# Optimization experiments

Measured on AMD Instinct MI355X. Metric: run time of the kernel, lower is better.

Reference implementation:

```python
import jax, jax.numpy as jnp
import numpy as np

N_HEADS = 4
DIM_HEAD = 32


def setup_inputs() -> dict:
    key = jax.random.key(0)
    k1, k2, k3, k4 = jax.random.split(key, 4)
    x = jax.random.normal(k1, (8, 64, 80, 1024), dtype=jnp.float32)
    # conv_qkv: 1x1 conv, no bias -> weight [3*heads*dim_head, dim_in_out]
    w_qkv = jax.random.normal(k2, (3 * N_HEADS * DIM_HEAD, 64), dtype=jnp.float32) * 0.05
    # conv_out: 1x1 conv with bias -> weight [dim_in_out, heads*dim_head], bias [dim_in_out]
    w_out = jax.random.normal(k3, (64, N_HEADS * DIM_HEAD), dtype=jnp.float32) * 0.05
    b_out = jax.random.normal(k4, (64,), dtype=jnp.float32) * 0.05
    return {"x": x, "w_qkv": w_qkv, "w_out": w_out, "b_out": b_out}


def reference(x, w_qkv, w_out, b_out):
    b, c, h, w = x.shape
    n = h * w
    # 1x1 conv == channel matmul
    qkv = jnp.einsum('bchw,oc->bohw', x, w_qkv)            # [b, 3*heads*dh, h, w]
    qkv = qkv.reshape(b, 3, N_HEADS, DIM_HEAD, n)          # qkv outermost, then heads, then c
    q, k, v = qkv[:, 0], qkv[:, 1], qkv[:, 2]              # each [b, heads, dh, n]
    k = jax.nn.softmax(k, axis=-1)                          # softmax over spatial positions
    context = jnp.einsum('bhdn,bhen->bhde', k, v)          # [b, heads, dh, dh]
    out = jnp.einsum('bhde,bhdn->bhen', context, q)        # [b, heads, dh, n]
    out = out.reshape(b, N_HEADS * DIM_HEAD, h, w)
    return jnp.einsum('bchw,oc->bohw', out, w_out) + b_out[None, :, None, None]
```

## Files before the change

kernel.cpp:

```cpp
#include <hip/hip_runtime.h>
#include <stdint.h>


#define N_POS 81920
#define NT    64
#define TILES 1280

typedef short bf16x8 __attribute__((ext_vector_type(8)));
typedef float f32x4  __attribute__((ext_vector_type(4)));

__device__ __forceinline__ uint32_t packbf(float lo, float hi){
  uint32_t a = __float_as_uint(lo), b = __float_as_uint(hi);
  a = (a + 0x8000u) >> 16;
  b = (b + 0x8000u) & 0xffff0000u;
  return a | b;
}
__device__ __forceinline__ short bf16of(float v){
  return (short)((__float_as_uint(v) + 0x8000u) >> 16);
}

__global__ __launch_bounds__(512, 4) void kernA(
    const float* __restrict__ x, const float* __restrict__ w,
    float* __restrict__ pA, float* __restrict__ pZ, int nch, int tpc)
{
  __shared__ __align__(16) uint16_t xs_cp[64 * 72];
  __shared__ __align__(16) uint16_t xs_pc[64 * 72];
  __shared__ __align__(16) uint16_t es[128 * 72];

  const int t  = threadIdx.x;
  const int w8 = t >> 6;
  const int l  = t & 63;
  const int lm = l & 15;
  const int lg = l >> 4;

  const int b  = blockIdx.x / nch;
  const int ch = blockIdx.x % nch;
  const float* xb = x + (size_t)b * 64 * N_POS;

  const int sc  = t >> 3;
  const int spg = t & 7;
  const int spp = t & 63;
  const int scg = t >> 6;

  const int pt  = w8 & 3;
  const int ht0 = (w8 >> 2) * 4;

  bf16x8 wkf[4][2];
  #pragma unroll
  for (int i = 0; i < 4; ++i)
    #pragma unroll
    for (int kk = 0; kk < 2; ++kk){
      const float* wp = w + (size_t)(128 + 16*(ht0+i) + lm) * 64 + 32*kk + 8*lg;
      float4 w0 = *(const float4*)wp;
      float4 w1 = *(const float4*)(wp + 4);
      bf16x8 f;
      f[0]=bf16of(w0.x); f[1]=bf16of(w0.y); f[2]=bf16of(w0.z); f[3]=bf16of(w0.w);
      f[4]=bf16of(w1.x); f[5]=bf16of(w1.y); f[6]=bf16of(w1.z); f[7]=bf16of(w1.w);
      wkf[i][kk] = f;
    }

  bf16x8 ones;
  #pragma unroll
  for (int j = 0; j < 8; ++j) ones[j] = (short)0x3F80;

  f32x4 acc[4], zac;
  zac = (f32x4){0.f,0.f,0.f,0.f};
  #pragma unroll
  for (int n = 0; n < 4; ++n) acc[n] = (f32x4){0.f,0.f,0.f,0.f};

  float4 f0, f1;
  float v[8];
  {
    const int n0 = (ch * tpc) * NT;
    const float* ga = xb + (size_t)sc * N_POS + n0 + 8*spg;
    f0 = *(const float4*)ga;
    f1 = *(const float4*)(ga + 4);
    const float* gb = xb + (size_t)(8*scg) * N_POS + n0 + spp;
    #pragma unroll
    for (int i = 0; i < 8; ++i) v[i] = gb[(size_t)i * N_POS];
  }

  for (int tile = 0; tile < tpc; ++tile){
    __syncthreads();
    {
      uint4 u;
      u.x = packbf(f0.x,f0.y); u.y = packbf(f0.z,f0.w);
      u.z = packbf(f1.x,f1.y); u.w = packbf(f1.z,f1.w);
      *(uint4*)&xs_cp[sc*72 + 8*spg] = u;
      uint4 u2;
      u2.x = packbf(v[0],v[1]); u2.y = packbf(v[2],v[3]);
      u2.z = packbf(v[4],v[5]); u2.w = packbf(v[6],v[7]);
      *(uint4*)&xs_pc[spp*72 + 8*scg] = u2;
    }
    __syncthreads();
    if (tile + 1 < tpc){
      const int n1 = (ch * tpc + tile + 1) * NT;
      const float* ga = xb + (size_t)sc * N_POS + n1 + 8*spg;
      f0 = *(const float4*)ga;
      f1 = *(const float4*)(ga + 4);
      const float* gb = xb + (size_t)(8*scg) * N_POS + n1 + spp;
      #pragma unroll
      for (int i = 0; i < 8; ++i) v[i] = gb[(size_t)i * N_POS];
    }
    {
      bf16x8 af0 = *(const bf16x8*)&xs_pc[(16*pt + lm)*72 + 8*lg];
      bf16x8 af1 = *(const bf16x8*)&xs_pc[(16*pt + lm)*72 + 32 + 8*lg];
      #pragma unroll
      for (int i = 0; i < 4; ++i){
        f32x4 s = (f32x4){0.f,0.f,0.f,0.f};
        s = __builtin_amdgcn_mfma_f32_16x16x32_bf16(af0, wkf[i][0], s, 0,0,0);
        s = __builtin_amdgcn_mfma_f32_16x16x32_bf16(af1, wkf[i][1], s, 0,0,0);
        float e0 = __expf(s[0]), e1 = __expf(s[1]);
        float e2 = __expf(s[2]), e3 = __expf(s[3]);
        uint2 pk; pk.x = packbf(e0,e1); pk.y = packbf(e2,e3);
        *(uint2*)&es[(16*(ht0+i) + lm)*72 + 16*pt + 4*lg] = pk;
      }
    }
    __syncthreads();
    #pragma unroll
    for (int kk = 0; kk < 2; ++kk){
      bf16x8 ea = *(const bf16x8*)&es[(16*w8 + lm)*72 + 32*kk + 8*lg];
      bf16x8 xbf[4];
      #pragma unroll
      for (int n = 0; n < 4; ++n)
        xbf[n] = *(const bf16x8*)&xs_cp[(16*n + lm)*72 + 32*kk + 8*lg];
      #pragma unroll
      for (int n = 0; n < 4; ++n)
        acc[n] = __builtin_amdgcn_mfma_f32_16x16x32_bf16(ea, xbf[n], acc[n], 0,0,0);
      zac = __builtin_amdgcn_mfma_f32_16x16x32_bf16(ea, ones, zac, 0,0,0);
    }
  }

  float* pa = pA + (size_t)blockIdx.x * 8192;
  const int hd0 = 16*w8 + 4*lg;
  #pragma unroll
  for (int n = 0; n < 4; ++n)
    #pragma unroll
    for (int r = 0; r < 4; ++r)
      pa[(size_t)(hd0 + r)*64 + 16*n + lm] = acc[n][r];
  if (lm == 0){
    #pragma unroll
    for (int r = 0; r < 4; ++r)
      pZ[(size_t)blockIdx.x * 128 + hd0 + r] = zac[r];
  }
}

__global__ __launch_bounds__(256) void kernR1(
    const float* __restrict__ pA, const float* __restrict__ pZ,
    float* __restrict__ Ar, float* __restrict__ Zr, int nch)
{
  const int b = blockIdx.x >> 3, s = blockIdx.x & 7;
  const int off = s * 1024 + threadIdx.x * 4;
  float4 a = make_float4(0.f, 0.f, 0.f, 0.f);
  for (int ch = 0; ch < nch; ++ch){
    float4 v = *(const float4*)&pA[(size_t)(b * nch + ch) * 8192 + off];
    a.x += v.x; a.y += v.y; a.z += v.z; a.w += v.w;
  }
  *(float4*)&Ar[(size_t)b * 8192 + off] = a;
  if (s == 0 && threadIdx.x < 128){
    float z = 0.f;
    for (int ch = 0; ch < nch; ++ch) z += pZ[(size_t)(b * nch + ch) * 128 + threadIdx.x];
    Zr[b * 128 + threadIdx.x] = z;
  }
}

__global__ __launch_bounds__(256) void kernCM(
    const float* __restrict__ Ar, const float* __restrict__ Zr,
    const float* __restrict__ w_qkv, const float* __restrict__ w_out,
    float* __restrict__ M)
{
  __shared__ float A[128 * 65];
  __shared__ float Z[128];
  __shared__ float cs[128 * 33];
  __shared__ float T[64 * 129];
  const int b = blockIdx.x, t = threadIdx.x;

  #pragma unroll
  for (int k = 0; k < 32; ++k){
    int i = t + 256 * k;
    A[(i >> 6) * 65 + (i & 63)] = Ar[(size_t)b * 8192 + i];
  }
  if (t < 128) Z[t] = Zr[b * 128 + t];
  __syncthreads();

  {
    const int hd = t & 127, h = hd >> 5, e0 = (t >> 7) * 16;
    const float rz = 1.0f / Z[hd];
    for (int je = 0; je < 16; ++je){
      int e = e0 + je;
      const float* wv = w_qkv + (size_t)(256 + 32 * h + e) * 64;
      float a = 0.f;
      #pragma unroll
      for (int c = 0; c < 64; ++c) a = fmaf(A[hd * 65 + c], wv[c], a);
      cs[hd * 33 + e] = a * rz;
    }
  }
  __syncthreads();

  const int o = t & 63, g = t >> 6;
  for (int jh = 0; jh < 32; ++jh){
    int hd = 32 * g + jh;
    const float* wo = w_out + (size_t)o * 128 + 32 * g;
    float a = 0.f;
    #pragma unroll
    for (int e = 0; e < 32; ++e) a = fmaf(wo[e], cs[hd * 33 + e], a);
    T[o * 129 + hd] = a;
  }
  __syncthreads();

  const int c0 = 16 * g;
  float m[16];
  #pragma unroll
  for (int j = 0; j < 16; ++j) m[j] = 0.f;
  for (int hd = 0; hd < 128; ++hd){
    float tv = T[o * 129 + hd];
    const float* wq = w_qkv + (size_t)hd * 64 + c0;
    #pragma unroll
    for (int j = 0; j < 16; ++j) m[j] = fmaf(tv, wq[j], m[j]);
  }
  #pragma unroll
  for (int j = 0; j < 16; ++j) M[(size_t)b * 4096 + o * 64 + c0 + j] = m[j];
}

__global__ __launch_bounds__(256, 2) void kernO(
    const float* __restrict__ x, const float* __restrict__ M,
    const float* __restrict__ b_out, float* __restrict__ out)
{
  __shared__ __align__(16) uint16_t xs[256 * 72];

  const int t  = threadIdx.x;
  const int wv = t >> 6;
  const int l  = t & 63;
  const int lm = l & 15;
  const int lg = l >> 4;

  const int b  = blockIdx.x / 320;
  const int p0 = (blockIdx.x % 320) * 256;
  const float* xb = x + (size_t)b * 64 * N_POS + p0;

  const float* Mb = M + (size_t)b * 4096;
  bf16x8 mb[4][2];
  float bias[4];
  #pragma unroll
  for (int ot = 0; ot < 4; ++ot){
    bias[ot] = b_out[16*ot + lm];
    #pragma unroll
    for (int kk = 0; kk < 2; ++kk){
      const float* mp = Mb + (size_t)(16*ot + lm)*64 + 32*kk + 8*lg;
      float4 m0 = *(const float4*)mp;
      float4 m1 = *(const float4*)(mp + 4);
      bf16x8 f;
      f[0]=bf16of(m0.x); f[1]=bf16of(m0.y); f[2]=bf16of(m0.z); f[3]=bf16of(m0.w);
      f[4]=bf16of(m1.x); f[5]=bf16of(m1.y); f[6]=bf16of(m1.z); f[7]=bf16of(m1.w);
      mb[ot][kk] = f;
    }
  }

  #pragma unroll
  for (int cc = 0; cc < 8; ++cc){
    float v[8];
    #pragma unroll
    for (int j = 0; j < 8; ++j)
      v[j] = xb[(size_t)(8*cc + j) * N_POS + t];
    uint4 u;
    u.x = packbf(v[0],v[1]); u.y = packbf(v[2],v[3]);
    u.z = packbf(v[4],v[5]); u.w = packbf(v[6],v[7]);
    *(uint4*)&xs[t*72 + 8*cc] = u;
  }
  __syncthreads();

  float* ob = out + (size_t)b * 64 * N_POS + p0;

  #pragma unroll
  for (int ip = 0; ip < 4; ++ip){
    const int pt = 4*wv + ip;
    bf16x8 af0 = *(const bf16x8*)&xs[(16*pt + lm)*72 + 8*lg];
    bf16x8 af1 = *(const bf16x8*)&xs[(16*pt + lm)*72 + 32 + 8*lg];
    #pragma unroll
    for (int ot = 0; ot < 4; ++ot){
      f32x4 d = (f32x4){0.f,0.f,0.f,0.f};
      d = __builtin_amdgcn_mfma_f32_16x16x32_bf16(af0, mb[ot][0], d, 0,0,0);
      d = __builtin_amdgcn_mfma_f32_16x16x32_bf16(af1, mb[ot][1], d, 0,0,0);
      float4 st = make_float4(d[0]+bias[ot], d[1]+bias[ot],
                              d[2]+bias[ot], d[3]+bias[ot]);
      *(float4*)&ob[(size_t)(16*ot + lm) * N_POS + 16*pt + 4*lg] = st;
    }
  }
}

extern "C" void kernel_launch(void* const* d_in, const int* in_sizes, int n_in,
                              void* d_out, int out_size, void* d_ws, size_t ws_size,
                              hipStream_t stream)
{
  const float* x     = (const float*)d_in[0];
  const float* w_qkv = (const float*)d_in[1];
  const float* w_out = (const float*)d_in[2];
  const float* b_out = (const float*)d_in[3];
  float* out = (float*)d_out;
  float* ws  = (float*)d_ws;

  static const int cand[] = {64, 40, 32, 20, 16, 10, 8, 5, 4, 2, 1};
  int nch = 1;
  for (int i = 0; i < 11; ++i){
    size_t need = ((size_t)8 * cand[i] * (8192 + 128)
                   + 8 * 8192 + 8 * 128 + (size_t)8 * 4096) * 4;
    if (need <= ws_size){ nch = cand[i]; break; }
  }
  const int tpc = TILES / nch;

  float* pA  = ws;
  float* pZ  = pA + (size_t)8 * nch * 8192;
  float* Ar  = pZ + (size_t)8 * nch * 128;
  float* Zr  = Ar + (size_t)8 * 8192;
  float* M   = Zr + (size_t)8 * 128;

  kernA<<<8 * nch, 512, 0, stream>>>(x, w_qkv, pA, pZ, nch, tpc);
  kernR1<<<64,     256, 0, stream>>>(pA, pZ, Ar, Zr, nch);
  kernCM<<<8,      256, 0, stream>>>(Ar, Zr, w_qkv, w_out, M);
  kernO<<<2560,    256, 0, stream>>>(x, M, b_out, out);
}
```

Baseline: 204.1 us.

## Double kernA position tile to 128 and raise MFMA priority and kernO occupancy

Widens the per-iteration spatial tile in the key-softmax/context kernel from 64 to 128 positions. Each thread now loads and packs twice as much, and each wave computes two position sub-tiles, which halves the number of barrier-separated iterations. The change also wraps the context MFMA loop in s_setprio so those waves get issue priority, and raises kernO's launch bounds to 4 blocks per SM. The cost is more LDS per block and more registers for prefetch, which may reduce kernA occupancy. kernO's register budget is also squeezed and could spill.

Result: no change. 204.0 us (-0.0%).

```diff
diff --git a/kernel.cpp b/kernel.cpp
--- a/kernel.cpp
+++ b/kernel.cpp
@@ -3,8 +3,8 @@
 
 
 #define N_POS 81920
-#define NT    64
-#define TILES 1280
+#define NT    128
+#define TILES 640
 
 typedef short bf16x8 __attribute__((ext_vector_type(8)));
 typedef float f32x4  __attribute__((ext_vector_type(4)));
@@ -23,9 +23,9 @@
     const float* __restrict__ x, const float* __restrict__ w,
     float* __restrict__ pA, float* __restrict__ pZ, int nch, int tpc)
 {
-  __shared__ __align__(16) uint16_t xs_cp[64 * 72];
-  __shared__ __align__(16) uint16_t xs_pc[64 * 72];
-  __shared__ __align__(16) uint16_t es[128 * 72];
+  __shared__ __align__(16) uint16_t xs_cp[64 * 136];
+  __shared__ __align__(16) uint16_t xs_pc[128 * 72];
+  __shared__ __align__(16) uint16_t es[128 * 136];
 
   const int t  = threadIdx.x;
   const int w8 = t >> 6;
@@ -37,12 +37,12 @@
   const int ch = blockIdx.x % nch;
   const float* xb = x + (size_t)b * 64 * N_POS;
 
-  const int sc  = t >> 3;
-  const int spg = t & 7;
-  const int spp = t & 63;
-  const int scg = t >> 6;
-
-  const int pt  = w8 & 3;
+  const int rr  = t >> 3;
+  const int pg  = t & 7;
+  const int spp = t & 127;
+  const int scg = t >> 7;
+
+  const int pth = w8 & 3;
   const int ht0 = (w8 >> 2) * 4;
 
   bf16x8 wkf[4][2];
@@ -68,41 +68,49 @@
   #pragma unroll
   for (int n = 0; n < 4; ++n) acc[n] = (f32x4){0.f,0.f,0.f,0.f};
 
-  float4 f0, f1;
-  float v[8];
+  float4 fa0, fa1, fa2, fa3;
+  float v[16];
   {
     const int n0 = (ch * tpc) * NT;
-    const float* ga = xb + (size_t)sc * N_POS + n0 + 8*spg;
-    f0 = *(const float4*)ga;
-    f1 = *(const float4*)(ga + 4);
-    const float* gb = xb + (size_t)(8*scg) * N_POS + n0 + spp;
-    #pragma unroll
-    for (int i = 0; i < 8; ++i) v[i] = gb[(size_t)i * N_POS];
+    const float* ga = xb + (size_t)rr * N_POS + n0 + 16*pg;
+    fa0 = *(const float4*)ga;       fa1 = *(const float4*)(ga + 4);
+    fa2 = *(const float4*)(ga + 8); fa3 = *(const float4*)(ga + 12);
+    const float* gb = xb + (size_t)(16*scg) * N_POS + n0 + spp;
+    #pragma unroll
+    for (int i = 0; i < 16; ++i) v[i] = gb[(size_t)i * N_POS];
   }
 
   for (int tile = 0; tile < tpc; ++tile){
     __syncthreads();
     {
-      uint4 u;
-      u.x = packbf(f0.x,f0.y); u.y = packbf(f0.z,f0.w);
-      u.z = packbf(f1.x,f1.y); u.w = packbf(f1.z,f1.w);
-      *(uint4*)&xs_cp[sc*72 + 8*spg] = u;
-      uint4 u2;
-      u2.x = packbf(v[0],v[1]); u2.y = packbf(v[2],v[3]);
-      u2.z = packbf(v[4],v[5]); u2.w = packbf(v[6],v[7]);
-      *(uint4*)&xs_pc[spp*72 + 8*scg] = u2;
+      uint4 u0, u1;
+      u0.x = packbf(fa0.x,fa0.y); u0.y = packbf(fa0.z,fa0.w);
+      u0.z = packbf(fa1.x,fa1.y); u0.w = packbf(fa1.z,fa1.w);
+      u1.x = packbf(fa2.x,fa2.y); u1.y = packbf(fa2.z,fa2.w);
+      u1.z = packbf(fa3.x,fa3.y); u1.w = packbf(fa3.z,fa3.w);
+      *(uint4*)&xs_cp[rr*136 + 16*pg]     = u0;
+      *(uint4*)&xs_cp[rr*136 + 16*pg + 8] = u1;
+      uint4 p0, p1;
+      p0.x = packbf(v[0],v[1]);   p0.y = packbf(v[2],v[3]);
+      p0.z = packbf(v[4],v[5]);   p0.w = packbf(v[6],v[7]);
+      p1.x = packbf(v[8],v[9]);   p1.y = packbf(v[10],v[11]);
+      p1.z = packbf(v[12],v[13]); p1.w = packbf(v[14],v[15]);
+      *(uint4*)&xs_pc[spp*72 + 16*scg]     = p0;
+      *(uint4*)&xs_pc[spp*72 + 16*scg + 8] = p1;
     }
     __syncthreads();
     if (tile + 1 < tpc){
       const int n1 = (ch * tpc + tile + 1) * NT;
-      const float* ga = xb + (size_t)sc * N_POS + n1 + 8*spg;
-      f0 = *(const float4*)ga;
-      f1 = *(const float4*)(ga + 4);
-      const float* gb = xb + (size_t)(8*scg) * N_POS + n1 + spp;
-      #pragma unroll
-      for (int i = 0; i < 8; ++i) v[i] = gb[(size_t)i * N_POS];
-    }
-    {
+      const float* ga = xb + (size_t)rr * N_POS + n1 + 16*pg;
+      fa0 = *(const float4*)ga;       fa1 = *(const float4*)(ga + 4);
+      fa2 = *(const float4*)(ga + 8); fa3 = *(const float4*)(ga + 12);
+      const float* gb = xb + (size_t)(16*scg) * N_POS + n1 + spp;
+      #pragma unroll
+      for (int i = 0; i < 16; ++i) v[i] = gb[(size_t)i * N_POS];
+    }
+    #pragma unroll
+    for (int ip = 0; ip < 2; ++ip){
+      const int pt = pth + 4*ip;
       bf16x8 af0 = *(const bf16x8*)&xs_pc[(16*pt + lm)*72 + 8*lg];
       bf16x8 af1 = *(const bf16x8*)&xs_pc[(16*pt + lm)*72 + 32 + 8*lg];
       #pragma unroll
@@ -113,22 +121,24 @@
         float e0 = __expf(s[0]), e1 = __expf(s[1]);
         float e2 = __expf(s[2]), e3 = __expf(s[3]);
         uint2 pk; pk.x = packbf(e0,e1); pk.y = packbf(e2,e3);
-        *(uint2*)&es[(16*(ht0+i) + lm)*72 + 16*pt + 4*lg] = pk;
+        *(uint2*)&es[(16*(ht0+i) + lm)*136 + 16*pt + 4*lg] = pk;
       }
     }
     __syncthreads();
-    #pragma unroll
-    for (int kk = 0; kk < 2; ++kk){
-      bf16x8 ea = *(const bf16x8*)&es[(16*w8 + lm)*72 + 32*kk + 8*lg];
+    __builtin_amdgcn_s_setprio(1);
+    #pragma unroll
+    for (int kk = 0; kk < 4; ++kk){
+      bf16x8 ea = *(const bf16x8*)&es[(16*w8 + lm)*136 + 32*kk + 8*lg];
       bf16x8 xbf[4];
       #pragma unroll
       for (int n = 0; n < 4; ++n)
-        xbf[n] = *(const bf16x8*)&xs_cp[(16*n + lm)*72 + 32*kk + 8*lg];
+        xbf[n] = *(const bf16x8*)&xs_cp[(16*n + lm)*136 + 32*kk + 8*lg];
       #pragma unroll
       for (int n = 0; n < 4; ++n)
         acc[n] = __builtin_amdgcn_mfma_f32_16x16x32_bf16(ea, xbf[n], acc[n], 0,0,0);
       zac = __builtin_amdgcn_mfma_f32_16x16x32_bf16(ea, ones, zac, 0,0,0);
     }
+    __builtin_amdgcn_s_setprio(0);
   }
 
   float* pa = pA + (size_t)blockIdx.x * 8192;
@@ -222,7 +232,7 @@
   for (int j = 0; j < 16; ++j) M[(size_t)b * 4096 + o * 64 + c0 + j] = m[j];
 }
 
-__global__ __launch_bounds__(256, 2) void kernO(
+__global__ __launch_bounds__(256, 4) void kernO(
     const float* __restrict__ x, const float* __restrict__ M,
     const float* __restrict__ b_out, float* __restrict__ out)
 {
```
